# Performance work log

Hardware: AMD Instinct MI355X
Metric: run time of the kernel (lower is better)

Reference implementation:

```python
import jax, jax.numpy as jnp
import numpy as np
from jax import lax

_DN = ('NCHW', 'OIHW', 'NCHW')
_EPS = 1e-5


def _conv3x3(x, w):
    return lax.conv_general_dilated(x, w, (1, 1), ((1, 1), (1, 1)), dimension_numbers=_DN)


def _bn(x, gamma, beta):
    # BatchNorm2d in (torch-default) training mode: batch statistics over (B,H,W)
    mean = x.mean(axis=(0, 2, 3), keepdims=True)
    var = x.var(axis=(0, 2, 3), keepdims=True)
    return (x - mean) * lax.rsqrt(var + _EPS) * gamma[None, :, None, None] + beta[None, :, None, None]


def _g1(x, w1, g1g, g1b, w2, g2g, g2b):
    x = jax.nn.relu(_bn(_conv3x3(x, w1), g1g, g1b))
    return jax.nn.relu(_bn(_conv3x3(x, w2), g2g, g2b))


def _weight_volume(left2, right2, maxdisp):
    # left2/right2: [B,1,H,W]. For each column j, min over window
    # [max(0, j-maxdisp), min(W, j+maxdisp)) of |right - left[:, :, :, j]|.
    L = left2[:, 0]  # [B,H,W]
    R = right2[:, 0]
    W = L.shape[-1]
    d = jnp.arange(-maxdisp, maxdisp)              # exclusive right bound -> offsets [-D, D-1]
    idx = jnp.arange(W)[:, None] + d[None, :]       # [W, 2D]
    valid = (idx >= 0) & (idx < W)
    g = R[:, :, jnp.clip(idx, 0, W - 1)]            # [B,H,W,2D]
    diff = jnp.where(valid, jnp.abs(g - L[..., None]), jnp.inf)
    v = diff.min(axis=-1)                           # [B,H,W]
    return (1.0 - jax.nn.sigmoid(v))[:, None]       # [B,1,H,W]


def setup_inputs() -> dict:
    key = jax.random.key(0)
    ks = jax.random.split(key, 5)
    B, C, H, W = 4, 32, 256, 512
    return {
        'left': jax.random.normal(ks[0], (B, C, H, W), jnp.float32),
        'right': jax.random.normal(ks[1], (B, C, H, W), jnp.float32),
        'w1': jax.random.normal(ks[2], (C, C, 3, 3), jnp.float32) * 0.05,
        'bn1_g': jnp.ones((C,), jnp.float32),
        'bn1_b': jnp.zeros((C,), jnp.float32),
        'w2': jax.random.normal(ks[3], (C, C, 3, 3), jnp.float32) * 0.05,
        'bn2_g': jnp.ones((C,), jnp.float32),
        'bn2_b': jnp.zeros((C,), jnp.float32),
        'g2_w': jax.random.normal(ks[4], (1, C, 1, 1), jnp.float32) * 0.1,
        'g2_b': jnp.zeros((1,), jnp.float32),
        'maxdisp': 48,
    }


def reference(left, right, w1, bn1_g, bn1_b, w2, bn2_g, bn2_b, g2_w, g2_b, maxdisp):
    left_g1 = _g1(left, w1, bn1_g, bn1_b, w2, bn2_g, bn2_b)
    right_g1 = _g1(right, w1, bn1_g, bn1_b, w2, bn2_g, bn2_b)
    # g2: 1x1 conv with bias -> single channel
    left_g2 = lax.conv_general_dilated(left_g1, g2_w, (1, 1), ((0, 0), (0, 0)), dimension_numbers=_DN) + g2_b[None, :, None, None]
    right_g2 = lax.conv_general_dilated(right_g1, g2_w, (1, 1), ((0, 0), (0, 0)), dimension_numbers=_DN) + g2_b[None, :, None, None]
    left_weight = _weight_volume(left_g2, right_g2, maxdisp)
    right_weight = _weight_volume(right_g2, left_g2, maxdisp)
    left_out = left_g1 * left_weight + left
    right_out = right_g1 * right_weight + right
    return (left_out, right_out)
```

## Files before the change

kernel.cpp:

```cpp
#include <hip/hip_runtime.h>

#define CC 32
#define HH 256
#define WW 512
#define HWSZ (HH*WW)
#define BB 4
#define NIMG 8
#define EPS 1e-5f
#define MAXD 48

#define ACT_R 10
#define ACT_C 66

typedef __attribute__((ext_vector_type(8))) short short8;
typedef __attribute__((ext_vector_type(4))) short short4v;
typedef __attribute__((ext_vector_type(16))) float f32x16;

__device__ inline unsigned short f2bf(float f) {
  unsigned int b = __builtin_bit_cast(unsigned int, f);
  b += 0x7FFFu + ((b >> 16) & 1u);
  return (unsigned short)(b >> 16);
}
__device__ inline float bf2f(short s) {
  unsigned int u = ((unsigned int)(unsigned short)s) << 16;
  return __builtin_bit_cast(float, u);
}

__global__ __launch_bounds__(256) void wxpose_k(
    const float* __restrict__ w1, const float* __restrict__ w2,
    short8* __restrict__ wtr)
{
  int e = blockIdx.x * 256 + threadIdx.x;
  if (e >= 2304) return;
  int which = e >= 1152;
  int i = e - which * 1152;
  const float* w = which ? w2 : w1;
  int ln = i & 31, lh = (i >> 5) & 1, t = (i >> 6) & 1, s = i >> 7;
  short8 v;
  #pragma unroll
  for (int j = 0; j < 8; ++j)
    v[j] = (short)f2bf(w[(size_t)(ln * CC + t * 16 + lh * 8 + j) * 9 + s]);
  wtr[e] = v;
}

__global__ __launch_bounds__(256) void xpose_k(
    const float* __restrict__ inL, const float* __restrict__ inR,
    short8* __restrict__ xin)
{
  const int img = blockIdx.x >> 8;
  const int y   = blockIdx.x & 255;
  const int g   = threadIdx.x >> 6;
  const int xl  = threadIdx.x & 63;
  const float* src = (img < BB ? inL : inR) + (size_t)(img & 3) * CC * HWSZ + (size_t)y * WW;
  short8* dst = xin + ((size_t)img * HH + y) * WW * 4;
  #pragma unroll
  for (int xc = 0; xc < 8; ++xc) {
    int x = xc * 64 + xl;
    short8 v;
    #pragma unroll
    for (int j = 0; j < 8; ++j)
      v[j] = (short)f2bf(src[(size_t)(g * 8 + j) * HWSZ + x]);
    dst[(size_t)x * 4 + g] = v;
  }
}

template<bool NORM>
__global__ __launch_bounds__(256, 3) void conv_k(
    const short8* __restrict__ xin, const short8* __restrict__ wtab,
    const float* __restrict__ scale, const float* __restrict__ shift,
    short8* __restrict__ yout, float* __restrict__ ssum, float* __restrict__ ssq)
{
  __shared__ short8 actb[4 * ACT_R * ACT_C];
  __shared__ float sred[256];

  const int tid  = threadIdx.x;
  const int img  = blockIdx.x >> 8;
  const int rem  = blockIdx.x & 255;
  const int y0   = (rem >> 3) * 8;
  const int x0   = (rem & 7) * 64;
  const int side = img >> 2;
  const int wid  = tid >> 6;
  const int lane = tid & 63;

  float scg[8], shg[8];
  if (NORM) {
    #pragma unroll
    for (int j = 0; j < 8; ++j) {
      scg[j] = scale[side * CC + wid * 8 + j];
      shg[j] = shift[side * CC + wid * 8 + j];
    }
  }

  const short8* srcimg = xin + (size_t)img * HH * WW * 4;
  #pragma unroll
  for (int i = 0; i < 11; ++i) {
    int e = lane + i * 64;
    if (e < ACT_R * ACT_C) {
      int r  = e / ACT_C;
      int c  = e - r * ACT_C;
      int yy = y0 - 1 + r;
      int xx = x0 - 1 + c;
      short8 v;
      if ((unsigned)yy < (unsigned)HH && (unsigned)xx < (unsigned)WW) {
        v = srcimg[((size_t)yy * WW + xx) * 4 + wid];
        if (NORM) {
          #pragma unroll
          for (int j = 0; j < 8; ++j) {
            float f = fmaxf(fmaf(bf2f(v[j]), scg[j], shg[j]), 0.f);
            v[j] = (short)f2bf(f);
          }
        }
      } else {
        #pragma unroll
        for (int j = 0; j < 8; ++j) v[j] = 0;
      }
      actb[(wid * ACT_R + r) * ACT_C + c] = v;
    }
  }
  __syncthreads();

  const int wr = wid >> 1;
  const int wc = wid & 1;
  const int lh = lane >> 5;
  const int ln = lane & 31;
  const int cbase = wc * 32 + ln;

  f32x16 acc[4];
  #pragma unroll
  for (int o = 0; o < 4; ++o)
    #pragma unroll
    for (int i = 0; i < 16; ++i) acc[o][i] = 0.f;

  #pragma unroll
  for (int t = 0; t < 2; ++t) {
    short8 afr[9];
    #pragma unroll
    for (int s = 0; s < 9; ++s)
      afr[s] = wtab[((s * 2 + t) * 2 + lh) * 32 + ln];
    #pragma unroll
    for (int irow = 0; irow < 6; ++irow) {
      const int rr = wr * 4 + irow;
      #pragma unroll
      for (int kx = 0; kx < 3; ++kx) {
        short8 b = actb[((t * 2 + lh) * ACT_R + rr) * ACT_C + cbase + kx];
        #pragma unroll
        for (int ky = 0; ky < 3; ++ky) {
          const int o = irow - ky;
          if (o >= 0 && o <= 3) {
            acc[o] = __builtin_amdgcn_mfma_f32_32x32x16_bf16(
                       afr[ky * 3 + kx], b, acc[o], 0, 0, 0);
          }
        }
      }
    }
  }

  const int ox = x0 + wc * 32 + ln;
  short4v* yb = (short4v*)yout;
  #pragma unroll
  for (int o = 0; o < 4; ++o) {
    const int oy = y0 + wr * 4 + o;
    const size_t pix = ((size_t)img * HH + oy) * WW + ox;
    #pragma unroll
    for (int qq = 0; qq < 4; ++qq) {
      short4v z;
      #pragma unroll
      for (int m = 0; m < 4; ++m) z[m] = (short)f2bf(acc[o][qq * 4 + m]);
      yb[pix * 8 + qq * 2 + lh] = z;
    }
  }

  float s16[16], q16[16];
  #pragma unroll
  for (int r16 = 0; r16 < 16; ++r16) {
    float s = 0.f, q = 0.f;
    #pragma unroll
    for (int o = 0; o < 4; ++o) { float v = acc[o][r16]; s += v; q += v * v; }
    #pragma unroll
    for (int off = 16; off >= 1; off >>= 1) {
      s += __shfl_xor(s, off);
      q += __shfl_xor(q, off);
    }
    s16[r16] = s; q16[r16] = q;
  }
  if (ln == 0) {
    #pragma unroll
    for (int r16 = 0; r16 < 16; ++r16) {
      const int co = (r16 & 3) + 8 * (r16 >> 2) + 4 * lh;
      sred[wid * 64 + co]      = s16[r16];
      sred[wid * 64 + 32 + co] = q16[r16];
    }
  }
  __syncthreads();
  if (tid < 64) {
    float v = sred[tid] + sred[64 + tid] + sred[128 + tid] + sred[192 + tid];
    if (tid < 32) atomicAdd(&ssum[side * CC + tid], v);
    else          atomicAdd(&ssq [side * CC + tid - 32], v);
  }
}

__global__ __launch_bounds__(64) void bnfin_k(
    const float* __restrict__ ssum, const float* __restrict__ ssq,
    const float* __restrict__ gamma, const float* __restrict__ beta,
    float* __restrict__ scale, float* __restrict__ shift)
{
  int t = threadIdx.x;
  int c = t & 31;
  const float n = (float)(BB * HWSZ);
  float m  = ssum[t] / n;
  float vr = ssq[t] / n - m * m;
  float sc = gamma[c] * rsqrtf(vr + EPS);
  scale[t] = sc;
  shift[t] = beta[c] - m * sc;
}

__global__ __launch_bounds__(256, 2) void ffinal_k(
    const short8* __restrict__ y2, const float* __restrict__ scale, const float* __restrict__ shift,
    const float* __restrict__ g2w, const float* __restrict__ g2b,
    const float* __restrict__ left, const float* __restrict__ right,
    float* __restrict__ out)
{
  __shared__ short8 zb[2][WW][4];
  __shared__ float g2r[2][WW];

  const int b   = blockIdx.x >> 8;
  const int h   = blockIdx.x & 255;
  const int tid = threadIdx.x;

  float wreg[32];
  #pragma unroll
  for (int g = 0; g < 8; ++g) {
    float4 t4 = *(const float4*)&g2w[g * 4];
    wreg[g * 4] = t4.x; wreg[g * 4 + 1] = t4.y; wreg[g * 4 + 2] = t4.z; wreg[g * 4 + 3] = t4.w;
  }
  const float g2b0 = g2b[0];

  #pragma unroll
  for (int side = 0; side < 2; ++side) {
    float scs[32], shs[32];
    #pragma unroll
    for (int g = 0; g < 8; ++g) {
      float4 a = *(const float4*)&scale[side * CC + g * 4];
      float4 c4 = *(const float4*)&shift[side * CC + g * 4];
      scs[g * 4] = a.x; scs[g * 4 + 1] = a.y; scs[g * 4 + 2] = a.z; scs[g * 4 + 3] = a.w;
      shs[g * 4] = c4.x; shs[g * 4 + 1] = c4.y; shs[g * 4 + 2] = c4.z; shs[g * 4 + 3] = c4.w;
    }
    const int img = side * BB + b;
    #pragma unroll
    for (int it = 0; it < 2; ++it) {
      const int x = it * 256 + tid;
      const size_t pixb = (((size_t)img * HH + h) * WW + x) * 4;
      float d = g2b0;
      #pragma unroll
      for (int g = 0; g < 4; ++g) {
        short8 v = y2[pixb + g];
        short8 z;
        #pragma unroll
        for (int j = 0; j < 8; ++j) {
          float f = fmaxf(fmaf(bf2f(v[j]), scs[g * 8 + j], shs[g * 8 + j]), 0.f);
          d += f * wreg[g * 8 + j];
          z[j] = (short)f2bf(f);
        }
        zb[side][x][g] = z;
      }
      g2r[side][x] = d;
    }
  }
  __syncthreads();

  const size_t OUT_R = (size_t)BB * CC * HWSZ;
  #pragma unroll
  for (int it = 0; it < 2; ++it) {
    const int x = it * 256 + tid;
    const float Lv = g2r[0][x], Rv = g2r[1][x];
    float vL = 1e30f, vR = 1e30f;
    const int lo = (x - MAXD < 0) ? 0 : (x - MAXD);
    const int hi = (x + MAXD - 1 > WW - 1) ? (WW - 1) : (x + MAXD - 1);
    for (int idx = lo; idx <= hi; ++idx) {
      vL = fminf(vL, fabsf(g2r[1][idx] - Lv));
      vR = fminf(vR, fabsf(g2r[0][idx] - Rv));
    }
    const float wL = 1.f / (1.f + __expf(vL));
    const float wR = 1.f / (1.f + __expf(vR));

    #pragma unroll
    for (int side = 0; side < 2; ++side) {
      const float wgt = side ? wR : wL;
      const float* inp = (side ? right : left) + (size_t)b * CC * HWSZ + (size_t)h * WW + x;
      float* op = out + (side ? OUT_R : 0) + (size_t)b * CC * HWSZ + (size_t)h * WW + x;
      short8 zz[4];
      #pragma unroll
      for (int g = 0; g < 4; ++g) zz[g] = zb[side][x][g];
      #pragma unroll
      for (int g = 0; g < 4; ++g)
        #pragma unroll
        for (int j = 0; j < 8; ++j) {
          const int c = g * 8 + j;
          op[(size_t)c * HWSZ] = bf2f(zz[g][j]) * wgt + inp[(size_t)c * HWSZ];
        }
    }
  }
}

extern "C" void kernel_launch(void* const* d_in, const int* in_sizes, int n_in,
                              void* d_out, int out_size, void* d_ws, size_t ws_size,
                              hipStream_t stream)
{
  const float* left  = (const float*)d_in[0];
  const float* right = (const float*)d_in[1];
  const float* w1    = (const float*)d_in[2];
  const float* bn1g  = (const float*)d_in[3];
  const float* bn1b  = (const float*)d_in[4];
  const float* w2    = (const float*)d_in[5];
  const float* bn2g  = (const float*)d_in[6];
  const float* bn2b  = (const float*)d_in[7];
  const float* g2w   = (const float*)d_in[8];
  const float* g2b   = (const float*)d_in[9];
  float* out = (float*)d_out;

  const size_t NB = (size_t)NIMG * HH * WW * 4;
  short8* xin = (short8*)d_ws;
  short8* y1  = xin + NB;
  short8* y2  = y1 + NB;
  short8* wtr = y2 + NB;
  float* stats = (float*)(wtr + 2304);

  float* sum1 = stats;       float* sq1 = stats + 64;
  float* sum2 = stats + 128; float* sq2 = stats + 192;
  float* sc1  = stats + 256; float* sh1 = stats + 320;
  float* sc2  = stats + 384; float* sh2 = stats + 448;

  hipMemsetAsync(stats, 0, 512 * sizeof(float), stream);

  wxpose_k<<<9, 256, 0, stream>>>(w1, w2, wtr);
  xpose_k<<<2048, 256, 0, stream>>>(left, right, xin);
  conv_k<false><<<2048, 256, 0, stream>>>(xin, wtr, nullptr, nullptr, y1, sum1, sq1);
  bnfin_k<<<1, 64, 0, stream>>>(sum1, sq1, bn1g, bn1b, sc1, sh1);
  conv_k<true><<<2048, 256, 0, stream>>>(y1, wtr + 1152, sc1, sh1, y2, sum2, sq2);
  bnfin_k<<<1, 64, 0, stream>>>(sum2, sq2, bn2g, bn2b, sc2, sh2);
  ffinal_k<<<1024, 256, 0, stream>>>(y2, sc2, sh2, g2w, g2b, left, right, out);
}
```

Measured before the change: 433.7 us.

## Load conv halo tiles via global_load_lds and split BN1 normalize into separate pass

```diff
diff --git a/kernel.cpp b/kernel.cpp
--- a/kernel.cpp
+++ b/kernel.cpp
@@ -11,10 +11,19 @@
 
 #define ACT_R 10
 #define ACT_C 66
+#define ACT_USED (ACT_R*ACT_C)
+#define ACT_STR 704
 
 typedef __attribute__((ext_vector_type(8))) short short8;
 typedef __attribute__((ext_vector_type(4))) short short4v;
 typedef __attribute__((ext_vector_type(16))) float f32x16;
+
+typedef __attribute__((address_space(1))) const unsigned int g_u32;
+typedef __attribute__((address_space(3))) unsigned int l_u32;
+
+__device__ __forceinline__ void gl_lds16(const void* g, void* l) {
+  __builtin_amdgcn_global_load_lds((g_u32*)g, (l_u32*)l, 16, 0, 0);
+}
 
 __device__ inline unsigned short f2bf(float f) {
   unsigned int b = __builtin_bit_cast(unsigned int, f);
@@ -64,14 +73,32 @@
   }
 }
 
-template<bool NORM>
+__global__ __launch_bounds__(256) void norm_k(
+    const short8* __restrict__ y, const float* __restrict__ scale,
+    const float* __restrict__ shift, short8* __restrict__ yn)
+{
+  const size_t tid = (size_t)blockIdx.x * 256 + threadIdx.x;
+  #pragma unroll
+  for (int k = 0; k < 8; ++k) {
+    const size_t p = (size_t)k * 524288 + tid;
+    const int side = (int)(p >> 21);
+    const int g    = (int)(p & 3);
+    const int cb   = side * CC + g * 8;
+    short8 v = y[p];
+    #pragma unroll
+    for (int j = 0; j < 8; ++j)
+      v[j] = (short)f2bf(fmaxf(fmaf(bf2f(v[j]), scale[cb + j], shift[cb + j]), 0.f));
+    yn[p] = v;
+  }
+}
+
 __global__ __launch_bounds__(256, 3) void conv_k(
     const short8* __restrict__ xin, const short8* __restrict__ wtab,
-    const float* __restrict__ scale, const float* __restrict__ shift,
+    const short8* __restrict__ zpage,
     short8* __restrict__ yout, float* __restrict__ ssum, float* __restrict__ ssq)
 {
-  __shared__ short8 actb[4 * ACT_R * ACT_C];
-  __shared__ float sred[256];
+  __shared__ short8 actb[4 * ACT_STR];
+  __shared__ float  sred[256];
 
   const int tid  = threadIdx.x;
   const int img  = blockIdx.x >> 8;
@@ -82,40 +109,17 @@
   const int wid  = tid >> 6;
   const int lane = tid & 63;
 
-  float scg[8], shg[8];
-  if (NORM) {
-    #pragma unroll
-    for (int j = 0; j < 8; ++j) {
-      scg[j] = scale[side * CC + wid * 8 + j];
-      shg[j] = shift[side * CC + wid * 8 + j];
-    }
-  }
-
   const short8* srcimg = xin + (size_t)img * HH * WW * 4;
   #pragma unroll
   for (int i = 0; i < 11; ++i) {
-    int e = lane + i * 64;
-    if (e < ACT_R * ACT_C) {
-      int r  = e / ACT_C;
-      int c  = e - r * ACT_C;
-      int yy = y0 - 1 + r;
-      int xx = x0 - 1 + c;
-      short8 v;
-      if ((unsigned)yy < (unsigned)HH && (unsigned)xx < (unsigned)WW) {
-        v = srcimg[((size_t)yy * WW + xx) * 4 + wid];
-        if (NORM) {
-          #pragma unroll
-          for (int j = 0; j < 8; ++j) {
-            float f = fmaxf(fmaf(bf2f(v[j]), scg[j], shg[j]), 0.f);
-            v[j] = (short)f2bf(f);
-          }
-        }
-      } else {
-        #pragma unroll
-        for (int j = 0; j < 8; ++j) v[j] = 0;
-      }
-      actb[(wid * ACT_R + r) * ACT_C + c] = v;
-    }
+    const int e = i * 64 + lane;
+    const int r = e / ACT_C;
+    const int c = e - r * ACT_C;
+    const int yy = y0 - 1 + r;
+    const int xx = x0 - 1 + c;
+    const bool ok = (e < ACT_USED) & ((unsigned)yy < (unsigned)HH) & ((unsigned)xx < (unsigned)WW);
+    const short8* src = ok ? &srcimg[((size_t)yy * WW + xx) * 4 + wid] : zpage;
+    gl_lds16(src, &actb[wid * ACT_STR + i * 64]);
   }
   __syncthreads();
 
@@ -142,7 +146,7 @@
       const int rr = wr * 4 + irow;
       #pragma unroll
       for (int kx = 0; kx < 3; ++kx) {
-        short8 b = actb[((t * 2 + lh) * ACT_R + rr) * ACT_C + cbase + kx];
+        short8 b = actb[(t * 2 + lh) * ACT_STR + rr * ACT_C + cbase + kx];
         #pragma unroll
         for (int ky = 0; ky < 3; ++ky) {
           const int o = irow - ky;
@@ -319,24 +323,27 @@
   float* out = (float*)d_out;
 
   const size_t NB = (size_t)NIMG * HH * WW * 4;
-  short8* xin = (short8*)d_ws;
-  short8* y1  = xin + NB;
-  short8* y2  = y1 + NB;
-  short8* wtr = y2 + NB;
+  short8* xin  = (short8*)d_ws;
+  short8* y1   = xin + NB;
+  short8* y1n  = y1 + NB;
+  short8* y2   = y1n + NB;
+  short8* wtr  = y2 + NB;
   float* stats = (float*)(wtr + 2304);
+  short8* zpage = (short8*)(stats + 512);
 
   float* sum1 = stats;       float* sq1 = stats + 64;
   float* sum2 = stats + 128; float* sq2 = stats + 192;
   float* sc1  = stats + 256; float* sh1 = stats + 320;
   float* sc2  = stats + 384; float* sh2 = stats + 448;
 
-  hipMemsetAsync(stats, 0, 512 * sizeof(float), stream);
+  hipMemsetAsync(stats, 0, 512 * sizeof(float) + 64, stream);
 
   wxpose_k<<<9, 256, 0, stream>>>(w1, w2, wtr);
   xpose_k<<<2048, 256, 0, stream>>>(left, right, xin);
-  conv_k<false><<<2048, 256, 0, stream>>>(xin, wtr, nullptr, nullptr, y1, sum1, sq1);
+  conv_k<<<2048, 256, 0, stream>>>(xin, wtr, zpage, y1, sum1, sq1);
   bnfin_k<<<1, 64, 0, stream>>>(sum1, sq1, bn1g, bn1b, sc1, sh1);
-  conv_k<true><<<2048, 256, 0, stream>>>(y1, wtr + 1152, sc1, sh1, y2, sum2, sq2);
+  norm_k<<<2048, 256, 0, stream>>>(y1, sc1, sh1, y1n);
+  conv_k<<<2048, 256, 0, stream>>>(y1n, wtr + 1152, zpage, y2, sum2, sq2);
   bnfin_k<<<1, 64, 0, stream>>>(sum2, sq2, bn2g, bn2b, sc2, sh2);
   ffinal_k<<<1024, 256, 0, stream>>>(y2, sc2, sh2, g2w, g2b, left, right, out);
 }
```

Measured after the change: 440.4 us. Within noise of the previous version (+1.5%).
